# Optimization experiments

Hardware: AMD Instinct MI355X
Metric: run time of the kernel (lower is better)

The kernel has to match this reference:

```python
import jax, jax.numpy as jnp
import numpy as np

C = 128
L = 4
NEG_SLOPE = 0.2


def _head(x, rb_w, rb_b, out_w, out_b):
    # x: [T, C]; rb_w: [2, 2, C, C] (block, layer) in torch Linear (out,in) layout.
    for i in range(2):
        h = jax.nn.leaky_relu(x @ rb_w[i, 0].T + rb_b[i, 0], NEG_SLOPE)
        h = h @ rb_w[i, 1].T + rb_b[i, 1]
        x = jax.nn.leaky_relu(x + h, NEG_SLOPE)  # act(shortcut + l2(act(l1(x))))
    return x @ out_w.T + out_b


def setup_inputs() -> dict:
    key = jax.random.key(0)
    ks = iter(jax.random.split(key, 32))
    s = 0.05  # small init so the relu-RNN recurrence stays stable over 32768 steps

    def w(shape):
        return jax.random.normal(next(ks), shape, jnp.float32) * s

    inp = {
        "x": jax.random.normal(next(ks), (C,), jnp.float32),
        "W_ih": w((L, C, C)),
        "W_hh": w((L, C, C)),
        "b_ih": w((L, C)),
        "b_hh": w((L, C)),
    }
    for name, out_dim in [("atom", 8), ("pos", 1), ("mag", 1)]:
        inp[name + "_rb_w"] = w((2, 2, C, C))
        inp[name + "_rb_b"] = w((2, 2, C))
        inp[name + "_w"] = w((out_dim, C))
        inp[name + "_b"] = w((out_dim,))
    inp["max_steps"] = 32768
    return inp


def reference(x, W_ih, W_hh, b_ih, b_hh,
              atom_rb_w, atom_rb_b, atom_w, atom_b,
              pos_rb_w, pos_rb_b, pos_w, pos_b,
              mag_rb_w, mag_rb_b, mag_w, mag_b,
              max_steps):
    # hid[0] = x (conditioning), other layers start at zero; first input is zeros.
    hid0 = jnp.zeros((L, C), x.dtype).at[0].set(x)
    inp0 = jnp.zeros((C,), x.dtype)

    def step(carry, _):
        xin, hid = carry  # xin: [C], hid: [L, C]
        cur = xin
        hs = []
        for l in range(L):
            cur = jax.nn.relu(cur @ W_ih[l].T + b_ih[l] + hid[l] @ W_hh[l].T + b_hh[l])
            hs.append(cur)
        new_hid = jnp.stack(hs)
        return (cur, new_hid), cur  # top-layer output is the next step's input

    _, encodings = jax.lax.scan(step, (inp0, hid0), None, length=max_steps)  # [T, C]

    atoms = _head(encodings, atom_rb_w, atom_rb_b, atom_w, atom_b)  # [T, 8]
    pos = _head(encodings, pos_rb_w, pos_rb_b, pos_w, pos_b)        # [T, 1]
    mags = _head(encodings, mag_rb_w, mag_rb_b, mag_w, mag_b)       # [T, 1]
    return jnp.concatenate([atoms, pos, mags], axis=-1)             # [T, 10]
```

## Files before the change

### kernel.cpp

```cpp
#include <hip/hip_runtime.h>
#include <cstdint>

typedef uint32_t u32;
typedef _Float16 f16;
typedef f16 f16x2 __attribute__((ext_vector_type(2)));
typedef f16 f16x8 __attribute__((ext_vector_type(8)));
typedef float f32x4 __attribute__((ext_vector_type(4)));

static __device__ __forceinline__ u32 pack2(float a, float b) {
    f16x2 v;
    v.x = (f16)a;
    v.y = (f16)b;
    return __builtin_bit_cast(u32, v);
}

static __device__ __forceinline__ float dot2(u32 a, u32 b, float c) {
    return __builtin_amdgcn_fdot2(__builtin_bit_cast(f16x2, a),
                                  __builtin_bit_cast(f16x2, b), c, false);
}

static __device__ __forceinline__ unsigned short f16bits(float v) {
    return __builtin_bit_cast(unsigned short, (f16)v);
}

static __device__ __forceinline__ float dpp_xor1_add(float v) {
    int x = __builtin_amdgcn_update_dpp(0, __builtin_bit_cast(int, v),
                                        0xB1, 0xF, 0xF, true);
    return v + __builtin_bit_cast(float, x);
}

#define BAR() asm volatile("s_waitcnt lgkmcnt(0)\n\ts_barrier" ::: "memory")

#define MFMA(A, B, C) __builtin_amdgcn_mfma_f32_16x16x32_f16(A, B, C, 0, 0, 0)

__global__ __launch_bounds__(512, 2) void rnn_kernel(
    const float* __restrict__ x0,
    const float* __restrict__ Wih, const float* __restrict__ Whh,
    const float* __restrict__ bih, const float* __restrict__ bhh,
    u32* __restrict__ enc, int T)
{
    __shared__ u32 buf[2][4][64];
    __shared__ float pre[4][128];

    const int tid  = threadIdx.x;
    const int wave = tid >> 6;
    const int lane = tid & 63;
    const int w    = wave & 3;

    const f32x4 ZERO4 = {0.f, 0.f, 0.f, 0.f};

    if (tid < 64)       buf[1][0][tid] = pack2(x0[2 * tid], x0[2 * tid + 1]);
    else if (tid < 256) ((u32*)buf[1])[tid] = 0u;
    __syncthreads();

    if (wave < 4) {
        const int rsh = w * 32 + (lane >> 1);
        const int kh  = lane & 1;

        u32 wih[4][32];
        float bsum[4];
        #pragma unroll
        for (int l = 0; l < 4; ++l) {
            const float* p = Wih + ((size_t)(l * 128 + rsh)) * 128 + kh * 64;
            #pragma unroll
            for (int j = 0; j < 32; ++j)
                wih[l][j] = pack2(p[2 * j], p[2 * j + 1]);
            bsum[l] = bih[l * 128 + rsh] + bhh[l * 128 + rsh];
        }
        BAR();

#define SLOT_IH(l, P, CURB, STORE, S) do {                                    \
        float pr = pre[l][rsh];                                               \
        const u32* _yb = (CURB) + kh * 32;                                    \
        uint4 h0 = *(const uint4*)(_yb + 0);                                  \
        uint4 h1 = *(const uint4*)(_yb + 4);                                  \
        uint4 h2 = *(const uint4*)(_yb + 8);                                  \
        uint4 h3 = *(const uint4*)(_yb + 12);                                 \
        uint4 h4 = *(const uint4*)(_yb + 16);                                 \
        uint4 h5 = *(const uint4*)(_yb + 20);                                 \
        uint4 h6 = *(const uint4*)(_yb + 24);                                 \
        uint4 h7 = *(const uint4*)(_yb + 28);                                 \
        const u32* _wd = wih[l];                                              \
        float va = kh ? 0.f : (pr + bsum[l]);                                 \
        float vb = 0.f, vc = 0.f, vd = 0.f;                                   \
        va = dot2(h0.x, _wd[0], va);  vb = dot2(h0.y, _wd[1], vb);            \
        vc = dot2(h0.z, _wd[2], vc);  vd = dot2(h0.w, _wd[3], vd);            \
        va = dot2(h1.x, _wd[4], va);  vb = dot2(h1.y, _wd[5], vb);            \
        vc = dot2(h1.z, _wd[6], vc);  vd = dot2(h1.w, _wd[7], vd);            \
        va = dot2(h2.x, _wd[8], va);  vb = dot2(h2.y, _wd[9], vb);            \
        vc = dot2(h2.z, _wd[10], vc); vd = dot2(h2.w, _wd[11], vd);           \
        va = dot2(h3.x, _wd[12], va); vb = dot2(h3.y, _wd[13], vb);           \
        vc = dot2(h3.z, _wd[14], vc); vd = dot2(h3.w, _wd[15], vd);           \
        va = dot2(h4.x, _wd[16], va); vb = dot2(h4.y, _wd[17], vb);           \
        vc = dot2(h4.z, _wd[18], vc); vd = dot2(h4.w, _wd[19], vd);           \
        va = dot2(h5.x, _wd[20], va); vb = dot2(h5.y, _wd[21], vb);           \
        vc = dot2(h5.z, _wd[22], vc); vd = dot2(h5.w, _wd[23], vd);           \
        va = dot2(h6.x, _wd[24], va); vb = dot2(h6.y, _wd[25], vb);           \
        vc = dot2(h6.z, _wd[26], vc); vd = dot2(h6.w, _wd[27], vd);           \
        va = dot2(h7.x, _wd[28], va); vb = dot2(h7.y, _wd[29], vb);           \
        vc = dot2(h7.z, _wd[30], vc); vd = dot2(h7.w, _wd[31], vd);           \
        float v = (va + vb) + (vc + vd);                                      \
        v = dpp_xor1_add(v);                                                  \
        float y = fmaxf(v, 0.f);                                              \
        if (kh == 0) {                                                        \
            unsigned short yb16 = f16bits(y);                                 \
            ((unsigned short*)&buf[P][l][0])[rsh] = yb16;                     \
            if (STORE)                                                        \
                ((unsigned short*)enc)[(size_t)(S) * 128 + rsh] = yb16;       \
        }                                                                     \
        BAR();                                                                \
    } while (0)

        for (int s = 0; s < T; s += 2) {
            SLOT_IH(0, 0, &buf[1][3][0], 0, s);
            SLOT_IH(1, 0, &buf[0][0][0], 0, s);
            SLOT_IH(2, 0, &buf[0][1][0], 0, s);
            SLOT_IH(3, 0, &buf[0][2][0], 1, s);
            SLOT_IH(0, 1, &buf[0][3][0], 0, s + 1);
            SLOT_IH(1, 1, &buf[1][0][0], 0, s + 1);
            SLOT_IH(2, 1, &buf[1][1][0], 0, s + 1);
            SLOT_IH(3, 1, &buf[1][2][0], 1, s + 1);
        }
#undef SLOT_IH
    } else {
        const int m = lane & 15;
        const int g = lane >> 4;

        f16x8 hhA[4][2][4];
        #pragma unroll
        for (int l = 0; l < 4; ++l)
            #pragma unroll
            for (int t = 0; t < 2; ++t) {
                const int row = w * 32 + t * 16 + m;
                #pragma unroll
                for (int kt = 0; kt < 4; ++kt) {
                    const float* p = Whh + ((size_t)(l * 128 + row)) * 128
                                         + kt * 32 + g * 8;
                    f16x8 v;
                    #pragma unroll
                    for (int e = 0; e < 8; ++e) v[e] = (f16)p[e];
                    hhA[l][t][kt] = v;
                }
            }

        f16x8 pfA[4], pfB[4];
        f32x4 pdA0, pdA1, pdB0, pdB1;

        {
            const u32* sb = &buf[1][0][0];
            f16x8 j0 = *(const f16x8*)(sb + 0 * 16 + g * 4);
            f16x8 j1 = *(const f16x8*)(sb + 1 * 16 + g * 4);
            f16x8 j2 = *(const f16x8*)(sb + 2 * 16 + g * 4);
            f16x8 j3 = *(const f16x8*)(sb + 3 * 16 + g * 4);
            f32x4 t0 = MFMA(hhA[0][0][0], j0, ZERO4);
            t0 = MFMA(hhA[0][0][1], j1, t0);
            t0 = MFMA(hhA[0][0][2], j2, t0);
            t0 = MFMA(hhA[0][0][3], j3, t0);
            f32x4 t1 = MFMA(hhA[0][1][0], j0, ZERO4);
            t1 = MFMA(hhA[0][1][1], j1, t1);
            t1 = MFMA(hhA[0][1][2], j2, t1);
            t1 = MFMA(hhA[0][1][3], j3, t1);
            if (m == 0) {
                *(f32x4*)&pre[0][w * 32 + g * 4] = t0;
                *(f32x4*)&pre[0][w * 32 + 16 + g * 4] = t1;
            }
            pdA0 = ZERO4;
            pdA1 = ZERO4;
            const u32* pb = &buf[1][2][0];
            #pragma unroll
            for (int kt = 0; kt < 4; ++kt)
                pfA[kt] = *(const f16x8*)(pb + kt * 16 + g * 4);
        }
        BAR();

#define SLOT_HH(LW, LC, PDW0, PDW1, PDN0, PDN1, PF_USE, PF_NEW, CURB) do {    \
        if (m == 0) {                                                         \
            *(f32x4*)&pre[LW][w * 32 + g * 4] = PDW0;                         \
            *(f32x4*)&pre[LW][w * 32 + 16 + g * 4] = PDW1;                    \
        }                                                                     \
        PDN0 = MFMA(hhA[LC][0][0], PF_USE[0], ZERO4);                         \
        PDN0 = MFMA(hhA[LC][0][1], PF_USE[1], PDN0);                          \
        PDN0 = MFMA(hhA[LC][0][2], PF_USE[2], PDN0);                          \
        PDN0 = MFMA(hhA[LC][0][3], PF_USE[3], PDN0);                          \
        PDN1 = MFMA(hhA[LC][1][0], PF_USE[0], ZERO4);                         \
        PDN1 = MFMA(hhA[LC][1][1], PF_USE[1], PDN1);                          \
        PDN1 = MFMA(hhA[LC][1][2], PF_USE[2], PDN1);                          \
        PDN1 = MFMA(hhA[LC][1][3], PF_USE[3], PDN1);                          \
        const u32* _pb = (CURB);                                              \
        PF_NEW[0] = *(const f16x8*)(_pb + 0 * 16 + g * 4);                    \
        PF_NEW[1] = *(const f16x8*)(_pb + 1 * 16 + g * 4);                    \
        PF_NEW[2] = *(const f16x8*)(_pb + 2 * 16 + g * 4);                    \
        PF_NEW[3] = *(const f16x8*)(_pb + 3 * 16 + g * 4);                    \
        BAR();                                                                \
    } while (0)

        for (int s = 0; s < T; s += 2) {
            SLOT_HH(1, 2, pdA0, pdA1, pdB0, pdB1, pfA, pfB, &buf[1][3][0]);
            SLOT_HH(2, 3, pdB0, pdB1, pdA0, pdA1, pfB, pfA, &buf[0][0][0]);
            SLOT_HH(3, 0, pdA0, pdA1, pdB0, pdB1, pfA, pfB, &buf[0][1][0]);
            SLOT_HH(0, 1, pdB0, pdB1, pdA0, pdA1, pfB, pfA, &buf[0][2][0]);
            SLOT_HH(1, 2, pdA0, pdA1, pdB0, pdB1, pfA, pfB, &buf[0][3][0]);
            SLOT_HH(2, 3, pdB0, pdB1, pdA0, pdA1, pfB, pfA, &buf[1][0][0]);
            SLOT_HH(3, 0, pdA0, pdA1, pdB0, pdB1, pfA, pfB, &buf[1][1][0]);
            SLOT_HH(0, 1, pdB0, pdB1, pdA0, pdA1, pfB, pfA, &buf[1][2][0]);
        }
#undef SLOT_HH
    }
}

__global__ __launch_bounds__(256) void heads_kernel(
    const u32* __restrict__ enc,
    const float* __restrict__ arw, const float* __restrict__ arb,
    const float* __restrict__ aw,  const float* __restrict__ ab,
    const float* __restrict__ prw, const float* __restrict__ prb,
    const float* __restrict__ pw,  const float* __restrict__ pb,
    const float* __restrict__ mrw, const float* __restrict__ mrb,
    const float* __restrict__ mw,  const float* __restrict__ mb,
    float* __restrict__ out, int T)
{
    const int head = blockIdx.x;
    const int r0 = blockIdx.y * 32;
    if (r0 >= T) return;

    const float *rbw, *rbb, *ow, *ob;
    int od, oc;
    if (head == 0)      { rbw = arw; rbb = arb; ow = aw; ob = ab; od = 8; oc = 0; }
    else if (head == 1) { rbw = prw; rbb = prb; ow = pw; ob = pb; od = 1; oc = 8; }
    else                { rbw = mrw; rbb = mrb; ow = mw; ob = mb; od = 1; oc = 9; }

    __shared__ u32 xs[32][64];
    __shared__ u32 hs[32][64];

    const int tid = threadIdx.x;

    #pragma unroll
    for (int rep = 0; rep < 8; ++rep) {
        int u = tid + rep * 256;
        int row = u >> 6, p = u & 63;
        xs[row][p] = enc[(size_t)(r0 + row) * 64 + p];
    }
    __syncthreads();

    const int j = tid & 127;
    const int rh = tid >> 7;

    float acc[16];
    u32 wreg[64];

#define PACKW(WPTR) do {                                                    \
        const float* _w = (WPTR);                                           \
        _Pragma("unroll")                                                   \
        for (int cc = 0; cc < 16; ++cc) {                                   \
            float4 aa = *(const float4*)(_w + cc * 8);                      \
            float4 bb = *(const float4*)(_w + cc * 8 + 4);                  \
            wreg[cc * 4 + 0] = pack2(aa.x, aa.y);                           \
            wreg[cc * 4 + 1] = pack2(aa.z, aa.w);                           \
            wreg[cc * 4 + 2] = pack2(bb.x, bb.y);                           \
            wreg[cc * 4 + 3] = pack2(bb.z, bb.w);                           \
        }                                                                   \
    } while (0)

#define MM16(SRC) do {                                                      \
        _Pragma("unroll")                                                   \
        for (int r = 0; r < 16; ++r) acc[r] = 0.f;                          \
        _Pragma("unroll")                                                   \
        for (int kp = 0; kp < 16; ++kp) {                                   \
            u32 w0 = wreg[kp * 4 + 0], w1 = wreg[kp * 4 + 1];               \
            u32 w2 = wreg[kp * 4 + 2], w3 = wreg[kp * 4 + 3];               \
            _Pragma("unroll")                                               \
            for (int r = 0; r < 16; ++r) {                                  \
                uint4 x4 = *(const uint4*)(&SRC[rh * 16 + r][kp * 4]);      \
                acc[r] = dot2(x4.x, w0, acc[r]);                            \
                acc[r] = dot2(x4.y, w1, acc[r]);                            \
                acc[r] = dot2(x4.z, w2, acc[r]);                            \
                acc[r] = dot2(x4.w, w3, acc[r]);                            \
            }                                                               \
        }                                                                   \
    } while (0)

    #pragma unroll
    for (int blk = 0; blk < 2; ++blk) {
        PACKW(rbw + (size_t)((blk * 2 + 0) * 128 + j) * 128);
        MM16(xs);
        {
            float b1 = rbb[(blk * 2 + 0) * 128 + j];
            #pragma unroll
            for (int r = 0; r < 16; ++r) {
                float v = acc[r] + b1;
                v = fmaxf(v, 0.2f * v);
                reinterpret_cast<unsigned short*>(&hs[rh * 16 + r][0])[j] = f16bits(v);
            }
        }
        __syncthreads();

        PACKW(rbw + (size_t)((blk * 2 + 1) * 128 + j) * 128);
        MM16(hs);
        {
            float b2 = rbb[(blk * 2 + 1) * 128 + j];
            #pragma unroll
            for (int r = 0; r < 16; ++r) {
                int row = rh * 16 + r;
                unsigned short xb =
                    reinterpret_cast<const unsigned short*>(&xs[row][0])[j];
                float xold = (float)__builtin_bit_cast(f16, xb);
                float v = xold + acc[r] + b2;
                v = fmaxf(v, 0.2f * v);
                reinterpret_cast<unsigned short*>(&xs[row][0])[j] = f16bits(v);
            }
        }
        __syncthreads();
    }

    {
        const int o = tid & 15;
        const int rr = tid >> 4;
        if (o < od) {
            PACKW(ow + (size_t)o * 128);
            float obv = ob[o];
            #pragma unroll
            for (int rs = 0; rs < 2; ++rs) {
                const int row = rr * 2 + rs;
                float a = 0.f;
                #pragma unroll
                for (int kp = 0; kp < 64; ++kp) a = dot2(xs[row][kp], wreg[kp], a);
                out[(size_t)(r0 + row) * 10 + oc + o] = a + obv;
            }
        }
    }
#undef PACKW
#undef MM16
}

extern "C" void kernel_launch(void* const* d_in, const int* in_sizes, int n_in,
                              void* d_out, int out_size, void* d_ws, size_t ws_size,
                              hipStream_t stream)
{
    const float* x   = (const float*)d_in[0];
    const float* Wih = (const float*)d_in[1];
    const float* Whh = (const float*)d_in[2];
    const float* bih = (const float*)d_in[3];
    const float* bhh = (const float*)d_in[4];
    const float* arw = (const float*)d_in[5];
    const float* arb = (const float*)d_in[6];
    const float* aw  = (const float*)d_in[7];
    const float* ab  = (const float*)d_in[8];
    const float* prw = (const float*)d_in[9];
    const float* prb = (const float*)d_in[10];
    const float* pw  = (const float*)d_in[11];
    const float* pb  = (const float*)d_in[12];
    const float* mrw = (const float*)d_in[13];
    const float* mrb = (const float*)d_in[14];
    const float* mw  = (const float*)d_in[15];
    const float* mb  = (const float*)d_in[16];

    const int T = out_size / 10;
    u32* enc = (u32*)d_ws;

    rnn_kernel<<<1, 512, 0, stream>>>(x, Wih, Whh, bih, bhh, enc, T);

    heads_kernel<<<dim3(3, (T + 31) / 32), 256, 0, stream>>>(
        enc, arw, arb, aw, ab, prw, prb, pw, pb, mrw, mrb, mw, mb,
        (float*)d_out, T);
}
```

Measured before the change: 35.50 ms.

## Merge input-path and recurrent-path waves into one 4-wave RNN block

The RNN kernel used 8 waves: four did the W_ih dot2 chain and four did the W_hh MFMA precompute, syncing through barriers each slot. Now each of four waves does both tasks in one slot, with a 256-thread block holding both weight sets in registers. This halves the waves taking part in every barrier and drops cross-wave handoff. In exchange each wave runs the dot2 chain and the MFMA work in sequence, and register pressure rises (wih plus hhA per thread), which may lengthen the serial step or cause spills.

```diff
diff --git a/kernel.cpp b/kernel.cpp
--- a/kernel.cpp
+++ b/kernel.cpp
@@ -33,7 +33,7 @@
 
 #define MFMA(A, B, C) __builtin_amdgcn_mfma_f32_16x16x32_f16(A, B, C, 0, 0, 0)
 
-__global__ __launch_bounds__(512, 2) void rnn_kernel(
+__global__ __launch_bounds__(256, 1) void rnn_kernel(
     const float* __restrict__ x0,
     const float* __restrict__ Wih, const float* __restrict__ Whh,
     const float* __restrict__ bih, const float* __restrict__ bhh,
@@ -43,33 +43,78 @@
     __shared__ float pre[4][128];
 
     const int tid  = threadIdx.x;
-    const int wave = tid >> 6;
+    const int w    = tid >> 6;
     const int lane = tid & 63;
-    const int w    = wave & 3;
+    const int rsh  = w * 32 + (lane >> 1);
+    const int kh   = lane & 1;
+    const int m    = lane & 15;
+    const int g    = lane >> 4;
 
     const f32x4 ZERO4 = {0.f, 0.f, 0.f, 0.f};
 
-    if (tid < 64)       buf[1][0][tid] = pack2(x0[2 * tid], x0[2 * tid + 1]);
-    else if (tid < 256) ((u32*)buf[1])[tid] = 0u;
+    u32 wih[4][32];
+    float bsum[4];
+    #pragma unroll
+    for (int l = 0; l < 4; ++l) {
+        const float* p = Wih + ((size_t)(l * 128 + rsh)) * 128 + kh * 64;
+        #pragma unroll
+        for (int j = 0; j < 32; ++j)
+            wih[l][j] = pack2(p[2 * j], p[2 * j + 1]);
+        bsum[l] = bih[l * 128 + rsh] + bhh[l * 128 + rsh];
+    }
+
+    f16x8 hhA[4][2][4];
+    #pragma unroll
+    for (int l = 0; l < 4; ++l)
+        #pragma unroll
+        for (int t = 0; t < 2; ++t) {
+            const int row = w * 32 + t * 16 + m;
+            #pragma unroll
+            for (int kt = 0; kt < 4; ++kt) {
+                const float* p = Whh + ((size_t)(l * 128 + row)) * 128
+                                     + kt * 32 + g * 8;
+                f16x8 v;
+                #pragma unroll
+                for (int e = 0; e < 8; ++e) v[e] = (f16)p[e];
+                hhA[l][t][kt] = v;
+            }
+        }
+
+    if (tid < 64) buf[1][0][tid] = pack2(x0[2 * tid], x0[2 * tid + 1]);
+    else          ((u32*)buf[1])[tid] = 0u;
     __syncthreads();
 
-    if (wave < 4) {
-        const int rsh = w * 32 + (lane >> 1);
-        const int kh  = lane & 1;
-
-        u32 wih[4][32];
-        float bsum[4];
+    f16x8 pfA[4], pfB[4];
+    f32x4 pdA0, pdA1, pdB0, pdB1;
+
+    {
+        const u32* sb = &buf[1][0][0];
+        f16x8 j0 = *(const f16x8*)(sb + 0 * 16 + g * 4);
+        f16x8 j1 = *(const f16x8*)(sb + 1 * 16 + g * 4);
+        f16x8 j2 = *(const f16x8*)(sb + 2 * 16 + g * 4);
+        f16x8 j3 = *(const f16x8*)(sb + 3 * 16 + g * 4);
+        f32x4 t0 = MFMA(hhA[0][0][0], j0, ZERO4);
+        t0 = MFMA(hhA[0][0][1], j1, t0);
+        t0 = MFMA(hhA[0][0][2], j2, t0);
+        t0 = MFMA(hhA[0][0][3], j3, t0);
+        f32x4 t1 = MFMA(hhA[0][1][0], j0, ZERO4);
+        t1 = MFMA(hhA[0][1][1], j1, t1);
+        t1 = MFMA(hhA[0][1][2], j2, t1);
+        t1 = MFMA(hhA[0][1][3], j3, t1);
+        if (m == 0) {
+            *(f32x4*)&pre[0][w * 32 + g * 4] = t0;
+            *(f32x4*)&pre[0][w * 32 + 16 + g * 4] = t1;
+        }
+        pdA0 = ZERO4;
+        pdA1 = ZERO4;
+        const u32* pb = &buf[1][2][0];
         #pragma unroll
-        for (int l = 0; l < 4; ++l) {
-            const float* p = Wih + ((size_t)(l * 128 + rsh)) * 128 + kh * 64;
-            #pragma unroll
-            for (int j = 0; j < 32; ++j)
-                wih[l][j] = pack2(p[2 * j], p[2 * j + 1]);
-            bsum[l] = bih[l * 128 + rsh] + bhh[l * 128 + rsh];
-        }
-        BAR();
-
-#define SLOT_IH(l, P, CURB, STORE, S) do {                                    \
+        for (int kt = 0; kt < 4; ++kt)
+            pfA[kt] = *(const f16x8*)(pb + kt * 16 + g * 4);
+    }
+
+#define SLOT(l, P, CURB, LW, LC, PDW0, PDW1, PDN0, PDN1, PF_USE, PF_NEW,      \
+             STORE, S) do {                                                   \
         float pr = pre[l][rsh];                                               \
         const u32* _yb = (CURB) + kh * 32;                                    \
         uint4 h0 = *(const uint4*)(_yb + 0);                                  \
@@ -80,6 +125,15 @@
         uint4 h5 = *(const uint4*)(_yb + 20);                                 \
         uint4 h6 = *(const uint4*)(_yb + 24);                                 \
         uint4 h7 = *(const uint4*)(_yb + 28);                                 \
+        const u32* _pb = (CURB);                                              \
+        PF_NEW[0] = *(const f16x8*)(_pb + 0 * 16 + g * 4);                    \
+        PF_NEW[1] = *(const f16x8*)(_pb + 1 * 16 + g * 4);                    \
+        PF_NEW[2] = *(const f16x8*)(_pb + 2 * 16 + g * 4);                    \
+        PF_NEW[3] = *(const f16x8*)(_pb + 3 * 16 + g * 4);                    \
+        if (m == 0) {                                                         \
+            *(f32x4*)&pre[LW][w * 32 + g * 4] = PDW0;                         \
+            *(f32x4*)&pre[LW][w * 32 + 16 + g * 4] = PDW1;                    \
+        }                                                                     \
         const u32* _wd = wih[l];                                              \
         float va = kh ? 0.f : (pr + bsum[l]);                                 \
         float vb = 0.f, vc = 0.f, vd = 0.f;                                   \
@@ -108,76 +162,6 @@
             if (STORE)                                                        \
                 ((unsigned short*)enc)[(size_t)(S) * 128 + rsh] = yb16;       \
         }                                                                     \
-        BAR();                                                                \
-    } while (0)
-
-        for (int s = 0; s < T; s += 2) {
-            SLOT_IH(0, 0, &buf[1][3][0], 0, s);
-            SLOT_IH(1, 0, &buf[0][0][0], 0, s);
-            SLOT_IH(2, 0, &buf[0][1][0], 0, s);
-            SLOT_IH(3, 0, &buf[0][2][0], 1, s);
-            SLOT_IH(0, 1, &buf[0][3][0], 0, s + 1);
-            SLOT_IH(1, 1, &buf[1][0][0], 0, s + 1);
-            SLOT_IH(2, 1, &buf[1][1][0], 0, s + 1);
-            SLOT_IH(3, 1, &buf[1][2][0], 1, s + 1);
-        }
-#undef SLOT_IH
-    } else {
-        const int m = lane & 15;
-        const int g = lane >> 4;
-
-        f16x8 hhA[4][2][4];
-        #pragma unroll
-        for (int l = 0; l < 4; ++l)
-            #pragma unroll
-            for (int t = 0; t < 2; ++t) {
-                const int row = w * 32 + t * 16 + m;
-                #pragma unroll
-                for (int kt = 0; kt < 4; ++kt) {
-                    const float* p = Whh + ((size_t)(l * 128 + row)) * 128
-                                         + kt * 32 + g * 8;
-                    f16x8 v;
-                    #pragma unroll
-                    for (int e = 0; e < 8; ++e) v[e] = (f16)p[e];
-                    hhA[l][t][kt] = v;
-                }
-            }
-
-        f16x8 pfA[4], pfB[4];
-        f32x4 pdA0, pdA1, pdB0, pdB1;
-
-        {
-            const u32* sb = &buf[1][0][0];
-            f16x8 j0 = *(const f16x8*)(sb + 0 * 16 + g * 4);
-            f16x8 j1 = *(const f16x8*)(sb + 1 * 16 + g * 4);
-            f16x8 j2 = *(const f16x8*)(sb + 2 * 16 + g * 4);
-            f16x8 j3 = *(const f16x8*)(sb + 3 * 16 + g * 4);
-            f32x4 t0 = MFMA(hhA[0][0][0], j0, ZERO4);
-            t0 = MFMA(hhA[0][0][1], j1, t0);
-            t0 = MFMA(hhA[0][0][2], j2, t0);
-            t0 = MFMA(hhA[0][0][3], j3, t0);
-            f32x4 t1 = MFMA(hhA[0][1][0], j0, ZERO4);
-            t1 = MFMA(hhA[0][1][1], j1, t1);
-            t1 = MFMA(hhA[0][1][2], j2, t1);
-            t1 = MFMA(hhA[0][1][3], j3, t1);
-            if (m == 0) {
-                *(f32x4*)&pre[0][w * 32 + g * 4] = t0;
-                *(f32x4*)&pre[0][w * 32 + 16 + g * 4] = t1;
-            }
-            pdA0 = ZERO4;
-            pdA1 = ZERO4;
-            const u32* pb = &buf[1][2][0];
-            #pragma unroll
-            for (int kt = 0; kt < 4; ++kt)
-                pfA[kt] = *(const f16x8*)(pb + kt * 16 + g * 4);
-        }
-        BAR();
-
-#define SLOT_HH(LW, LC, PDW0, PDW1, PDN0, PDN1, PF_USE, PF_NEW, CURB) do {    \
-        if (m == 0) {                                                         \
-            *(f32x4*)&pre[LW][w * 32 + g * 4] = PDW0;                         \
-            *(f32x4*)&pre[LW][w * 32 + 16 + g * 4] = PDW1;                    \
-        }                                                                     \
         PDN0 = MFMA(hhA[LC][0][0], PF_USE[0], ZERO4);                         \
         PDN0 = MFMA(hhA[LC][0][1], PF_USE[1], PDN0);                          \
         PDN0 = MFMA(hhA[LC][0][2], PF_USE[2], PDN0);                          \
@@ -186,26 +170,20 @@
         PDN1 = MFMA(hhA[LC][1][1], PF_USE[1], PDN1);                          \
         PDN1 = MFMA(hhA[LC][1][2], PF_USE[2], PDN1);                          \
         PDN1 = MFMA(hhA[LC][1][3], PF_USE[3], PDN1);                          \
-        const u32* _pb = (CURB);                                              \
-        PF_NEW[0] = *(const f16x8*)(_pb + 0 * 16 + g * 4);                    \
-        PF_NEW[1] = *(const f16x8*)(_pb + 1 * 16 + g * 4);                    \
-        PF_NEW[2] = *(const f16x8*)(_pb + 2 * 16 + g * 4);                    \
-        PF_NEW[3] = *(const f16x8*)(_pb + 3 * 16 + g * 4);                    \
         BAR();                                                                \
     } while (0)
 
-        for (int s = 0; s < T; s += 2) {
-            SLOT_HH(1, 2, pdA0, pdA1, pdB0, pdB1, pfA, pfB, &buf[1][3][0]);
-            SLOT_HH(2, 3, pdB0, pdB1, pdA0, pdA1, pfB, pfA, &buf[0][0][0]);
-            SLOT_HH(3, 0, pdA0, pdA1, pdB0, pdB1, pfA, pfB, &buf[0][1][0]);
-            SLOT_HH(0, 1, pdB0, pdB1, pdA0, pdA1, pfB, pfA, &buf[0][2][0]);
-            SLOT_HH(1, 2, pdA0, pdA1, pdB0, pdB1, pfA, pfB, &buf[0][3][0]);
-            SLOT_HH(2, 3, pdB0, pdB1, pdA0, pdA1, pfB, pfA, &buf[1][0][0]);
-            SLOT_HH(3, 0, pdA0, pdA1, pdB0, pdB1, pfA, pfB, &buf[1][1][0]);
-            SLOT_HH(0, 1, pdB0, pdB1, pdA0, pdA1, pfB, pfA, &buf[1][2][0]);
-        }
-#undef SLOT_HH
-    }
+    for (int s = 0; s < T; s += 2) {
+        SLOT(0, 0, &buf[1][3][0], 1, 2, pdA0, pdA1, pdB0, pdB1, pfA, pfB, 0, s);
+        SLOT(1, 0, &buf[0][0][0], 2, 3, pdB0, pdB1, pdA0, pdA1, pfB, pfA, 0, s);
+        SLOT(2, 0, &buf[0][1][0], 3, 0, pdA0, pdA1, pdB0, pdB1, pfA, pfB, 0, s);
+        SLOT(3, 0, &buf[0][2][0], 0, 1, pdB0, pdB1, pdA0, pdA1, pfB, pfA, 1, s);
+        SLOT(0, 1, &buf[0][3][0], 1, 2, pdA0, pdA1, pdB0, pdB1, pfA, pfB, 0, s + 1);
+        SLOT(1, 1, &buf[1][0][0], 2, 3, pdB0, pdB1, pdA0, pdA1, pfB, pfA, 0, s + 1);
+        SLOT(2, 1, &buf[1][1][0], 3, 0, pdA0, pdA1, pdB0, pdB1, pfA, pfB, 0, s + 1);
+        SLOT(3, 1, &buf[1][2][0], 0, 1, pdB0, pdB1, pdA0, pdA1, pfB, pfA, 1, s + 1);
+    }
+#undef SLOT
 }
 
 __global__ __launch_bounds__(256) void heads_kernel(
@@ -356,7 +334,7 @@
     const int T = out_size / 10;
     u32* enc = (u32*)d_ws;
 
-    rnn_kernel<<<1, 512, 0, stream>>>(x, Wih, Whh, bih, bhh, enc, T);
+    rnn_kernel<<<1, 256, 0, stream>>>(x, Wih, Whh, bih, bhh, enc, T);
 
     heads_kernel<<<dim3(3, (T + 31) / 32), 256, 0, stream>>>(
         enc, arw, arb, aw, ab, prw, prb, pw, pb, mrw, mrb, mw, mb,
```

Result: slower. 48.06 ms (+35.4%).
